# Kernel tuning notes

Hardware: AMD Instinct MI355X
Metric: run time of the kernel (lower is better)

Reference implementation:

```python
import jax, jax.numpy as jnp
import numpy as np

N = 262144          # total neurons (num_neurons * batch_size)
S = 4194304         # total synapses (~16 per neuron)
L = 8               # delay ring-buffer length (steps)
DT = 1e-4
SLOPE = 4.0
T_NOW = 0.0
# uniform per-neuron params (original stores them via _full(const))
SOMA_C, SOMA_GL, SOMA_EL = 2e-10, 1e-8, -0.070
AIS_C, AIS_GL, AIS_EL = 1e-10, 1e-8, -0.070
V_T, DELTA_T, V_SPIKE, V_RESET = -0.050, 0.002, -0.030, -0.065
G_C = 5e-9
# uniform per-synapse params (tiled constants in connect())
G_MAX, E_REV, TAU_DECAY = 1e-9, 0.0, 0.005
A_PLUS, A_MINUS, TAU_PRE, TAU_POST = 0.01, 0.012, 0.020, 0.020
ETA_BCM, TAU_RATE, TAU_THETA = 1e-4, 0.100, 1.000
W_MIN, W_MAX = 0.0, 1.0


def setup_inputs() -> dict:
    key = jax.random.key(0)
    ks = jax.random.split(key, 14)
    return {
        "external_current": 2e-10 * jax.random.normal(ks[0], (N,), jnp.float32),
        "syn_w": jax.random.uniform(ks[1], (S,), jnp.float32),
        "V_soma": SOMA_EL + 0.005 * jax.random.normal(ks[2], (N,), jnp.float32),
        "V_ais": -0.050 + 0.030 * jax.random.normal(ks[3], (N,), jnp.float32),
        "refrac_until": jnp.full((N,), -1e9, jnp.float32),
        "syn_g": 0.5 * jax.random.uniform(ks[4], (S,), jnp.float32),
        "pre_trace": jax.random.uniform(ks[5], (S,), jnp.float32),
        "post_trace": jax.random.uniform(ks[6], (S,), jnp.float32),
        "r_pre": jax.random.uniform(ks[7], (S,), jnp.float32),
        "r_post": jax.random.uniform(ks[8], (S,), jnp.float32),
        "theta_m": jax.random.uniform(ks[9], (S,), jnp.float32),
        "g_incr_buffer": jnp.zeros((L, S), jnp.float32),
        "syn_pre_idx": jax.random.randint(ks[10], (S,), 0, N, jnp.int32),
        "syn_post_idx": jax.random.randint(ks[11], (S,), 0, N, jnp.int32),
        "delay_steps": jax.random.randint(ks[12], (S,), 1, L, jnp.int32),
        "buffer_idx": 0,
    }


def reference(external_current, syn_w, V_soma, V_ais, refrac_until, syn_g,
              pre_trace, post_trace, r_pre, r_post, theta_m,
              g_incr_buffer, syn_pre_idx, syn_post_idx, delay_steps, buffer_idx):
    n = V_soma.shape[0]
    # conductance-based synaptic current, gathered from post voltage, scattered to post neurons
    i_syn = syn_g * syn_w * G_MAX * (E_REV - V_soma[syn_post_idx])
    I_syn_total = jax.ops.segment_sum(i_syn, syn_post_idx, num_segments=n)
    # two-compartment step (explicit Euler): passive soma + AdEx AIS, coupled by g_c
    dvs = (DT / SOMA_C) * (-SOMA_GL * (V_soma - SOMA_EL) + external_current
                           + I_syn_total + G_C * (V_ais - V_soma))
    exp_term = AIS_GL * DELTA_T * jnp.exp(jnp.minimum((V_ais - V_T) / DELTA_T, 20.0))
    dva = (DT / AIS_C) * (-AIS_GL * (V_ais - AIS_EL) + exp_term + G_C * (V_soma - V_ais))
    V_soma_new = V_soma + dvs
    V_ais_new = jnp.where(T_NOW < refrac_until, V_RESET, V_ais + dva)
    # spike detection with sigmoid surrogate gradient
    hard = (V_ais_new >= V_SPIKE).astype(V_ais_new.dtype)
    soft = jax.nn.sigmoid(SLOPE * (V_ais_new - V_SPIKE))
    spikes = soft + jax.lax.stop_gradient(hard - soft)
    V_ais_out = jnp.where(hard > 0, V_RESET, V_ais_new)
    # conductance: exponential decay + delayed arrivals read from ring buffer slot
    arrivals = g_incr_buffer[buffer_idx]
    syn_g_new = syn_g * jnp.exp(-DT / TAU_DECAY) + arrivals
    pre_spk = spikes[syn_pre_idx]
    post_spk = spikes[syn_post_idx]
    # schedule this step's pre-spikes at per-synapse delay slots; clear consumed slot
    rows = (buffer_idx + delay_steps) % L
    buf_new = g_incr_buffer.at[buffer_idx].set(0.0).at[rows, jnp.arange(syn_w.shape[0])].add(pre_spk)
    # STDP eligibility traces
    pre_tr = pre_trace * jnp.exp(-DT / TAU_PRE) + pre_spk
    post_tr = post_trace * jnp.exp(-DT / TAU_POST) + post_spk
    dw_stdp = A_PLUS * pre_tr * post_spk - A_MINUS * post_tr * pre_spk
    # BCM low-pass rates and sliding threshold
    r_pre_n = r_pre * jnp.exp(-DT / TAU_RATE) + pre_spk
    r_post_n = r_post * jnp.exp(-DT / TAU_RATE) + post_spk
    theta_n = theta_m + (DT / TAU_THETA) * (r_post_n * r_post_n - theta_m)
    dw_bcm = ETA_BCM * r_pre_n * r_post_n * (r_post_n - theta_n)
    w_new = jnp.clip(syn_w + dw_stdp + dw_bcm, W_MIN, W_MAX)
    return (spikes, V_soma_new, V_ais_out, syn_g_new, w_new, buf_new)
```

## Files before the change

kernel.cpp:

```cpp
#include <hip/hip_runtime.h>
#include <math.h>

#define C_DT_OVER_SOMA  500000.0f
#define C_DT_OVER_AIS   1000000.0f
#define C_SOMA_GL       1e-8f
#define C_SOMA_EL       (-0.070f)
#define C_AIS_GL        1e-8f
#define C_AIS_EL        (-0.070f)
#define C_V_T           (-0.050f)
#define C_DELTA_T       0.002f
#define C_V_SPIKE       (-0.030f)
#define C_V_RESET       (-0.065f)
#define C_G_C           5e-9f
#define C_G_MAX         1e-9f
#define C_DECAY_G       0.9801986733067553f
#define C_DECAY_TR      0.9950124791926823f
#define C_DECAY_RATE    0.9990004998333751f
#define C_DT_TAU_THETA  1e-4f
#define C_A_PLUS        0.01f
#define C_A_MINUS       0.012f
#define C_ETA_BCM       1e-4f

#define TILE_BITS   15
#define TILE_SIZE   32768
#define TILE_MASK   (TILE_SIZE - 1)
#define NTILES      8
#define KCHUNK      32
#define RING_BPR    256

typedef float fx4 __attribute__((ext_vector_type(4)));
typedef unsigned char uchar;

__device__ __forceinline__ fx4 nt_load4(const float* p) {
    return __builtin_nontemporal_load((const fx4*)p);
}
__device__ __forceinline__ void nt_store4(float* p, fx4 v) {
    __builtin_nontemporal_store(v, (fx4*)p);
}

__global__ void k_zero4(float4* __restrict__ p, int n4) {
    int i = blockIdx.x * blockDim.x + threadIdx.x;
    if (i < n4) p[i] = make_float4(0.f, 0.f, 0.f, 0.f);
}

__global__ void __launch_bounds__(512, 1)
k_scatter_tile(const float4* __restrict__ g4,
               const float4* __restrict__ w4,
               const int4*   __restrict__ post4,
               float*        __restrict__ partials,
               int S) {
    extern __shared__ float acc[];
    const int t = blockIdx.x & (NTILES - 1);
    const int k = blockIdx.x >> 3;

    for (int i = threadIdx.x; i < TILE_SIZE; i += blockDim.x)
        acc[i] = 0.0f;
    __syncthreads();

    const int cnt4  = (S / KCHUNK) / 4;
    const int base4 = k * cnt4;
    for (int j = threadIdx.x; j < cnt4; j += blockDim.x) {
        int4   p = post4[base4 + j];
        float4 g = g4[base4 + j];
        float4 w = w4[base4 + j];
        if ((p.x >> TILE_BITS) == t) atomicAdd(&acc[p.x & TILE_MASK], g.x * w.x);
        if ((p.y >> TILE_BITS) == t) atomicAdd(&acc[p.y & TILE_MASK], g.y * w.y);
        if ((p.z >> TILE_BITS) == t) atomicAdd(&acc[p.z & TILE_MASK], g.z * w.z);
        if ((p.w >> TILE_BITS) == t) atomicAdd(&acc[p.w & TILE_MASK], g.w * w.w);
    }
    __syncthreads();

    float4* dst = (float4*)(partials + (size_t)blockIdx.x * TILE_SIZE);
    const float4* src = (const float4*)acc;
    for (int i = threadIdx.x; i < TILE_SIZE / 4; i += blockDim.x)
        dst[i] = src[i];
}

template <bool FAST>
__global__ void k_neuron(const float* __restrict__ ext,
                         const float* __restrict__ Vs,
                         const float* __restrict__ Va,
                         const float* __restrict__ refrac,
                         const float* __restrict__ A,
                         float* __restrict__ spikes,
                         float* __restrict__ Vs_out,
                         float* __restrict__ Va_out,
                         int N) {
    int i = blockIdx.x * blockDim.x + threadIdx.x;
    if (i >= N) return;
    float acc = 0.0f;
    if (FAST) {
        const int t = i >> TILE_BITS;
        const int local = i & TILE_MASK;
        const float* base = A + ((size_t)t * KCHUNK) * TILE_SIZE + local;
        #pragma unroll
        for (int k = 0; k < KCHUNK; ++k) acc += base[(size_t)k * TILE_SIZE];
    } else {
        acc = A[i];
    }
    float vs = Vs[i];
    float va = Va[i];
    float I_syn = C_G_MAX * (0.0f - vs) * acc;
    float dvs = C_DT_OVER_SOMA * (-C_SOMA_GL * (vs - C_SOMA_EL) + ext[i]
                                  + I_syn + C_G_C * (va - vs));
    float xarg = fminf((va - C_V_T) / C_DELTA_T, 20.0f);
    float exp_term = C_AIS_GL * C_DELTA_T * expf(xarg);
    float dva = C_DT_OVER_AIS * (-C_AIS_GL * (va - C_AIS_EL) + exp_term
                                 + C_G_C * (vs - va));
    float vs_new = vs + dvs;
    float va_new = (0.0f < refrac[i]) ? C_V_RESET : (va + dva);
    float hard = (va_new >= C_V_SPIKE) ? 1.0f : 0.0f;
    float va_out = (hard > 0.0f) ? C_V_RESET : va_new;
    spikes[i] = hard;
    __builtin_nontemporal_store(vs_new, &Vs_out[i]);
    __builtin_nontemporal_store(va_out, &Va_out[i]);
}

__global__ void k_bits(const float* __restrict__ spikes,
                       unsigned long long* __restrict__ bits,
                       int N) {
    int i = blockIdx.x * blockDim.x + threadIdx.x;
    if (i >= N) return;
    float s = spikes[i];
    unsigned long long m = __ballot(s > 0.5f);
    if ((threadIdx.x & 63) == 0) bits[i >> 6] = m;
}

__global__ void k_scatter_gw_dev(const float4* __restrict__ g4,
                                 const float4* __restrict__ w4,
                                 const int4*   __restrict__ post4,
                                 float*        __restrict__ A,
                                 int S4) {
    int t = blockIdx.x * blockDim.x + threadIdx.x;
    if (t >= S4) return;
    float4 g = g4[t];
    float4 w = w4[t];
    int4   p = post4[t];
    unsafeAtomicAdd(&A[p.x], g.x * w.x);
    unsafeAtomicAdd(&A[p.y], g.y * w.y);
    unsafeAtomicAdd(&A[p.z], g.z * w.z);
    unsafeAtomicAdd(&A[p.w], g.w * w.w);
}

__device__ __forceinline__ float bit_gather(const unsigned* __restrict__ bits32, int idx) {
    return (float)((bits32[idx >> 5] >> (idx & 31)) & 1u);
}

__global__ void k_plast_bits(const float* __restrict__ syn_w,
                             const float* __restrict__ pre_trace,
                             const float* __restrict__ post_trace,
                             const float* __restrict__ r_pre,
                             const float* __restrict__ r_post,
                             const float* __restrict__ theta_m,
                             const int*   __restrict__ pre_idx,
                             const int*   __restrict__ post_idx,
                             const int*   __restrict__ delay,
                             const int*   __restrict__ bidx_p,
                             const unsigned* __restrict__ bits32,
                             float* __restrict__ w_out,
                             uchar* __restrict__ prerow,
                             int S) {
    int t = blockIdx.x * blockDim.x + threadIdx.x;
    int j = t * 8;
    if (j >= S) return;
    const int bidx = bidx_p[0];

    int4 pi0 = *(const int4*)(pre_idx + j);
    int4 pi1 = *(const int4*)(pre_idx + j + 4);
    int4 qi0 = *(const int4*)(post_idx + j);
    int4 qi1 = *(const int4*)(post_idx + j + 4);
    int4 dl0 = *(const int4*)(delay + j);
    int4 dl1 = *(const int4*)(delay + j + 4);

    float pre[8], post[8];
    pre[0] = bit_gather(bits32, pi0.x); pre[1] = bit_gather(bits32, pi0.y);
    pre[2] = bit_gather(bits32, pi0.z); pre[3] = bit_gather(bits32, pi0.w);
    pre[4] = bit_gather(bits32, pi1.x); pre[5] = bit_gather(bits32, pi1.y);
    pre[6] = bit_gather(bits32, pi1.z); pre[7] = bit_gather(bits32, pi1.w);
    post[0] = bit_gather(bits32, qi0.x); post[1] = bit_gather(bits32, qi0.y);
    post[2] = bit_gather(bits32, qi0.z); post[3] = bit_gather(bits32, qi0.w);
    post[4] = bit_gather(bits32, qi1.x); post[5] = bit_gather(bits32, qi1.y);
    post[6] = bit_gather(bits32, qi1.z); post[7] = bit_gather(bits32, qi1.w);

    float4 w0  = *(const float4*)(syn_w + j);
    float4 w1  = *(const float4*)(syn_w + j + 4);
    float4 pt0 = *(const float4*)(pre_trace + j);
    float4 pt1 = *(const float4*)(pre_trace + j + 4);
    float4 qt0 = *(const float4*)(post_trace + j);
    float4 qt1 = *(const float4*)(post_trace + j + 4);
    float4 rp0 = *(const float4*)(r_pre + j);
    float4 rp1 = *(const float4*)(r_pre + j + 4);
    float4 rq0 = *(const float4*)(r_post + j);
    float4 rq1 = *(const float4*)(r_post + j + 4);
    float4 th0 = *(const float4*)(theta_m + j);
    float4 th1 = *(const float4*)(theta_m + j + 4);

    float wv[8]  = {w0.x, w0.y, w0.z, w0.w, w1.x, w1.y, w1.z, w1.w};
    float ptv[8] = {pt0.x, pt0.y, pt0.z, pt0.w, pt1.x, pt1.y, pt1.z, pt1.w};
    float qtv[8] = {qt0.x, qt0.y, qt0.z, qt0.w, qt1.x, qt1.y, qt1.z, qt1.w};
    float rpv[8] = {rp0.x, rp0.y, rp0.z, rp0.w, rp1.x, rp1.y, rp1.z, rp1.w};
    float rqv[8] = {rq0.x, rq0.y, rq0.z, rq0.w, rq1.x, rq1.y, rq1.z, rq1.w};
    float thv[8] = {th0.x, th0.y, th0.z, th0.w, th1.x, th1.y, th1.z, th1.w};
    int   dlv[8] = {dl0.x, dl0.y, dl0.z, dl0.w, dl1.x, dl1.y, dl1.z, dl1.w};

    float wo[8];
    unsigned prw[8];
    #pragma unroll
    for (int k = 0; k < 8; ++k) {
        float ptr_n = ptv[k] * C_DECAY_TR + pre[k];
        float qtr_n = qtv[k] * C_DECAY_TR + post[k];
        float dw_stdp = C_A_PLUS * ptr_n * post[k] - C_A_MINUS * qtr_n * pre[k];
        float rpn = rpv[k] * C_DECAY_RATE + pre[k];
        float rqn = rqv[k] * C_DECAY_RATE + post[k];
        float thn = thv[k] + C_DT_TAU_THETA * (rqn * rqn - thv[k]);
        float dw_bcm = C_ETA_BCM * rpn * rqn * (rqn - thn);
        float wn = wv[k] + dw_stdp + dw_bcm;
        wo[k] = fminf(fmaxf(wn, 0.0f), 1.0f);
        prw[k] = (pre[k] > 0.5f) ? (unsigned)(((bidx + dlv[k]) & 7) + 1) : 0u;
    }
    fx4 a = {wo[0], wo[1], wo[2], wo[3]};
    fx4 b = {wo[4], wo[5], wo[6], wo[7]};
    nt_store4(w_out + j, a);
    nt_store4(w_out + j + 4, b);

    uint2 packed;
    packed.x = prw[0] | (prw[1] << 8) | (prw[2] << 16) | (prw[3] << 24);
    packed.y = prw[4] | (prw[5] << 8) | (prw[6] << 16) | (prw[7] << 24);
    *(uint2*)(prerow + j) = packed;
}

__global__ void k_ring_row(const float* __restrict__ gbuf,
                           const float* __restrict__ syn_g,
                           const uchar* __restrict__ prerow,
                           const int*   __restrict__ bidx_p,
                           float* __restrict__ g_out,
                           float* __restrict__ buf_out,
                           int S) {
    const int bidx = bidx_p[0];
    const int row  = blockIdx.x / RING_BPR;
    const int blk  = blockIdx.x - row * RING_BPR;
    const int span = S / RING_BPR;
    const int base = blk * span;
    const float* src = gbuf + (size_t)row * (size_t)S;
    float*       dst = buf_out + (size_t)row * (size_t)S;
    const unsigned target = (unsigned)(row + 1);
    const int step = blockDim.x * 4;

    if (row == bidx) {
        for (int off = threadIdx.x * 4; off < span; off += step) {
            const int j = base + off;
            fx4 v  = nt_load4(src + j);
            fx4 sg = *(const fx4*)(syn_g + j);
            fx4 go = sg * (float)C_DECAY_G + v;
            nt_store4(g_out + j, go);
            unsigned wd = *(const unsigned*)(prerow + j);
            fx4 z;
            z.x = ((wd        & 255u) == target) ? 1.0f : 0.0f;
            z.y = (((wd >> 8)  & 255u) == target) ? 1.0f : 0.0f;
            z.z = (((wd >> 16) & 255u) == target) ? 1.0f : 0.0f;
            z.w = (((wd >> 24)       ) == target) ? 1.0f : 0.0f;
            nt_store4(dst + j, z);
        }
    } else {
        for (int off = threadIdx.x * 4; off < span; off += step) {
            const int j = base + off;
            fx4 v = nt_load4(src + j);
            unsigned wd = *(const unsigned*)(prerow + j);
            v.x += ((wd        & 255u) == target) ? 1.0f : 0.0f;
            v.y += (((wd >> 8)  & 255u) == target) ? 1.0f : 0.0f;
            v.z += (((wd >> 16) & 255u) == target) ? 1.0f : 0.0f;
            v.w += (((wd >> 24)       ) == target) ? 1.0f : 0.0f;
            nt_store4(dst + j, v);
        }
    }
}

__global__ void k_syn_update4(const float* __restrict__ syn_g,
                              const float* __restrict__ syn_w,
                              const float* __restrict__ pre_trace,
                              const float* __restrict__ post_trace,
                              const float* __restrict__ r_pre,
                              const float* __restrict__ r_post,
                              const float* __restrict__ theta_m,
                              const float* __restrict__ gbuf,
                              const int*   __restrict__ pre_idx,
                              const int*   __restrict__ post_idx,
                              const int*   __restrict__ delay,
                              const int*   __restrict__ bidx_p,
                              const float* __restrict__ spikes,
                              float* __restrict__ g_out,
                              float* __restrict__ w_out,
                              float* __restrict__ buf_out,
                              int S, int L) {
    int t = blockIdx.x * blockDim.x + threadIdx.x;
    int j = t * 4;
    if (j >= S) return;
    const int bidx = bidx_p[0];
    int4 pi = *(const int4*)(pre_idx + j);
    int4 qi = *(const int4*)(post_idx + j);
    int4 dl = *(const int4*)(delay + j);
    float pre[4], post[4];
    pre[0] = spikes[pi.x]; pre[1] = spikes[pi.y]; pre[2] = spikes[pi.z]; pre[3] = spikes[pi.w];
    post[0] = spikes[qi.x]; post[1] = spikes[qi.y]; post[2] = spikes[qi.z]; post[3] = spikes[qi.w];
    float4 g  = *(const float4*)(syn_g + j);
    float4 w  = *(const float4*)(syn_w + j);
    float4 pt = *(const float4*)(pre_trace + j);
    float4 qt = *(const float4*)(post_trace + j);
    float4 rp = *(const float4*)(r_pre + j);
    float4 rq = *(const float4*)(r_post + j);
    float4 th = *(const float4*)(theta_m + j);
    float wv[4]  = {w.x, w.y, w.z, w.w};
    float ptv[4] = {pt.x, pt.y, pt.z, pt.w};
    float qtv[4] = {qt.x, qt.y, qt.z, qt.w};
    float rpv[4] = {rp.x, rp.y, rp.z, rp.w};
    float rqv[4] = {rq.x, rq.y, rq.z, rq.w};
    float thv[4] = {th.x, th.y, th.z, th.w};
    float wo[4];
    #pragma unroll
    for (int k = 0; k < 4; ++k) {
        float ptr_n = ptv[k] * C_DECAY_TR + pre[k];
        float qtr_n = qtv[k] * C_DECAY_TR + post[k];
        float dw_stdp = C_A_PLUS * ptr_n * post[k] - C_A_MINUS * qtr_n * pre[k];
        float rpn = rpv[k] * C_DECAY_RATE + pre[k];
        float rqn = rqv[k] * C_DECAY_RATE + post[k];
        float thn = thv[k] + C_DT_TAU_THETA * (rqn * rqn - thv[k]);
        float dw_bcm = C_ETA_BCM * rpn * rqn * (rqn - thn);
        float wn = wv[k] + dw_stdp + dw_bcm;
        wo[k] = fminf(fmaxf(wn, 0.0f), 1.0f);
    }
    float4 wo4 = {wo[0], wo[1], wo[2], wo[3]};
    *(float4*)(w_out + j) = wo4;
    int row[4];
    row[0] = (bidx + dl.x) % L;
    row[1] = (bidx + dl.y) % L;
    row[2] = (bidx + dl.z) % L;
    row[3] = (bidx + dl.w) % L;
    float gv[4] = {g.x, g.y, g.z, g.w};
    for (int r = 0; r < L; ++r) {
        float4 v = *(const float4*)(gbuf + (size_t)r * (size_t)S + j);
        float vv[4] = {v.x, v.y, v.z, v.w};
        if (r == bidx) {
            float4 gn;
            gn.x = gv[0] * C_DECAY_G + vv[0];
            gn.y = gv[1] * C_DECAY_G + vv[1];
            gn.z = gv[2] * C_DECAY_G + vv[2];
            gn.w = gv[3] * C_DECAY_G + vv[3];
            *(float4*)(g_out + j) = gn;
            vv[0] = vv[1] = vv[2] = vv[3] = 0.0f;
        }
        #pragma unroll
        for (int k = 0; k < 4; ++k)
            if (r == row[k]) vv[k] += pre[k];
        float4 ov = {vv[0], vv[1], vv[2], vv[3]};
        *(float4*)(buf_out + (size_t)r * (size_t)S + j) = ov;
    }
}

extern "C" void kernel_launch(void* const* d_in, const int* in_sizes, int n_in,
                              void* d_out, int out_size, void* d_ws, size_t ws_size,
                              hipStream_t stream) {
    const int N = in_sizes[0];
    const int S = in_sizes[1];
    const int L = in_sizes[11] / S;

    const float* ext        = (const float*)d_in[0];
    const float* syn_w      = (const float*)d_in[1];
    const float* Vs         = (const float*)d_in[2];
    const float* Va         = (const float*)d_in[3];
    const float* refrac     = (const float*)d_in[4];
    const float* syn_g      = (const float*)d_in[5];
    const float* pre_trace  = (const float*)d_in[6];
    const float* post_trace = (const float*)d_in[7];
    const float* r_pre      = (const float*)d_in[8];
    const float* r_post     = (const float*)d_in[9];
    const float* theta_m    = (const float*)d_in[10];
    const float* gbuf       = (const float*)d_in[11];
    const int*   pre_idx    = (const int*)d_in[12];
    const int*   post_idx   = (const int*)d_in[13];
    const int*   delay      = (const int*)d_in[14];
    const int*   bidx       = (const int*)d_in[15];

    float* out     = (float*)d_out;
    float* spikes  = out;
    float* Vs_out  = out + (size_t)N;
    float* Va_out  = out + (size_t)2 * N;
    float* g_out   = out + (size_t)3 * N;
    float* w_out   = out + (size_t)3 * N + (size_t)S;
    float* buf_out = out + (size_t)3 * N + (size_t)2 * S;

    float* A = (float*)d_ws;
    uchar* prerow = (uchar*)d_ws;
    unsigned long long* bits = (unsigned long long*)((char*)d_ws + ((size_t)8 << 20));

    const size_t need = (size_t)NTILES * KCHUNK * TILE_SIZE * sizeof(float);
    const bool fastScatter = (N == NTILES * TILE_SIZE) &&
                             (S % (KCHUNK * 4) == 0) &&
                             (ws_size >= need);
    const bool fastSyn = fastScatter && (L == 8) && (S % (RING_BPR * 256 * 4) == 0) &&
                         (S % 8 == 0) && (N % 256 == 0) &&
                         (((size_t)8 << 20) + N / 8 <= ws_size) && ((size_t)S <= ((size_t)8 << 20));

    const int B = 256;
    if (fastScatter) {
        k_scatter_tile<<<NTILES * KCHUNK, 512, TILE_SIZE * sizeof(float), stream>>>(
            (const float4*)syn_g, (const float4*)syn_w, (const int4*)post_idx, A, S);
        k_neuron<true><<<(N + B - 1) / B, B, 0, stream>>>(ext, Vs, Va, refrac, A,
                                                          spikes, Vs_out, Va_out, N);
    } else {
        const int S4 = S / 4;
        k_zero4<<<(N / 4 + B - 1) / B, B, 0, stream>>>((float4*)A, N / 4);
        k_scatter_gw_dev<<<(S4 + B - 1) / B, B, 0, stream>>>((const float4*)syn_g,
                                                             (const float4*)syn_w,
                                                             (const int4*)post_idx, A, S4);
        k_neuron<false><<<(N + B - 1) / B, B, 0, stream>>>(ext, Vs, Va, refrac, A,
                                                           spikes, Vs_out, Va_out, N);
    }

    if (fastSyn) {
        k_bits<<<N / B, B, 0, stream>>>(spikes, bits, N);
        const int T8 = S / 8;
        k_plast_bits<<<(T8 + B - 1) / B, B, 0, stream>>>(syn_w, pre_trace, post_trace,
                                                         r_pre, r_post, theta_m,
                                                         pre_idx, post_idx, delay, bidx,
                                                         (const unsigned*)bits,
                                                         w_out, prerow, S);
        k_ring_row<<<8 * RING_BPR, B, 0, stream>>>(gbuf, syn_g, prerow, bidx,
                                                   g_out, buf_out, S);
    } else {
        const int T4 = (S + 3) / 4;
        k_syn_update4<<<(T4 + B - 1) / B, B, 0, stream>>>(syn_g, syn_w, pre_trace, post_trace,
                                                          r_pre, r_post, theta_m, gbuf,
                                                          pre_idx, post_idx, delay, bidx,
                                                          spikes, g_out, w_out, buf_out, S, L);
    }
}
```

Measured before the change: 158.0 us.

## Stage spike bitmask in LDS, use nontemporal streaming loads, reorder scatter tile grid

The plasticity kernel now copies the whole 32 KB spike bitmask into shared memory per block, so the 16 random pre/post spike lookups hit LDS instead of global memory. Streaming per-synapse loads (indices, delays, weights, traces, syn_g, partial sums) use nontemporal hints to reduce cache pollution. The scatter-tile grid mapping is changed so consecutive blocks share a tile, with partials written to the same layout. The price is a 32 KB LDS fill per plasticity block, which may lower occupancy and add redundant global reads.

After: 181.4 us. +14.8%, slower.

```diff
diff --git a/kernel.cpp b/kernel.cpp
--- a/kernel.cpp
+++ b/kernel.cpp
@@ -27,12 +27,20 @@
 #define NTILES      8
 #define KCHUNK      32
 #define RING_BPR    256
+#define NBW         8192
 
 typedef float fx4 __attribute__((ext_vector_type(4)));
+typedef int   ix4 __attribute__((ext_vector_type(4)));
 typedef unsigned char uchar;
 
 __device__ __forceinline__ fx4 nt_load4(const float* p) {
     return __builtin_nontemporal_load((const fx4*)p);
+}
+__device__ __forceinline__ ix4 nt_loadi4(const int* p) {
+    return __builtin_nontemporal_load((const ix4*)p);
+}
+__device__ __forceinline__ float nt_loadf(const float* p) {
+    return __builtin_nontemporal_load(p);
 }
 __device__ __forceinline__ void nt_store4(float* p, fx4 v) {
     __builtin_nontemporal_store(v, (fx4*)p);
@@ -50,8 +58,8 @@
                float*        __restrict__ partials,
                int S) {
     extern __shared__ float acc[];
-    const int t = blockIdx.x & (NTILES - 1);
-    const int k = blockIdx.x >> 3;
+    const int t = blockIdx.x >> 5;
+    const int k = blockIdx.x & 31;
 
     for (int i = threadIdx.x; i < TILE_SIZE; i += blockDim.x)
         acc[i] = 0.0f;
@@ -70,10 +78,10 @@
     }
     __syncthreads();
 
-    float4* dst = (float4*)(partials + (size_t)blockIdx.x * TILE_SIZE);
+    float* dst = partials + ((size_t)t * KCHUNK + k) * TILE_SIZE;
     const float4* src = (const float4*)acc;
     for (int i = threadIdx.x; i < TILE_SIZE / 4; i += blockDim.x)
-        dst[i] = src[i];
+        ((float4*)dst)[i] = src[i];
 }
 
 template <bool FAST>
@@ -94,7 +102,7 @@
         const int local = i & TILE_MASK;
         const float* base = A + ((size_t)t * KCHUNK) * TILE_SIZE + local;
         #pragma unroll
-        for (int k = 0; k < KCHUNK; ++k) acc += base[(size_t)k * TILE_SIZE];
+        for (int k = 0; k < KCHUNK; ++k) acc += nt_loadf(base + (size_t)k * TILE_SIZE);
     } else {
         acc = A[i];
     }
@@ -142,10 +150,6 @@
     unsafeAtomicAdd(&A[p.w], g.w * w.w);
 }
 
-__device__ __forceinline__ float bit_gather(const unsigned* __restrict__ bits32, int idx) {
-    return (float)((bits32[idx >> 5] >> (idx & 31)) & 1u);
-}
-
 __global__ void k_plast_bits(const float* __restrict__ syn_w,
                              const float* __restrict__ pre_trace,
                              const float* __restrict__ post_trace,
@@ -160,40 +164,46 @@
                              float* __restrict__ w_out,
                              uchar* __restrict__ prerow,
                              int S) {
+    __shared__ unsigned sb[NBW];
+    for (int i = threadIdx.x; i < NBW; i += blockDim.x)
+        sb[i] = bits32[i];
+    __syncthreads();
+
     int t = blockIdx.x * blockDim.x + threadIdx.x;
     int j = t * 8;
     if (j >= S) return;
     const int bidx = bidx_p[0];
 
-    int4 pi0 = *(const int4*)(pre_idx + j);
-    int4 pi1 = *(const int4*)(pre_idx + j + 4);
-    int4 qi0 = *(const int4*)(post_idx + j);
-    int4 qi1 = *(const int4*)(post_idx + j + 4);
-    int4 dl0 = *(const int4*)(delay + j);
-    int4 dl1 = *(const int4*)(delay + j + 4);
+    ix4 pi0 = nt_loadi4(pre_idx + j);
+    ix4 pi1 = nt_loadi4(pre_idx + j + 4);
+    ix4 qi0 = nt_loadi4(post_idx + j);
+    ix4 qi1 = nt_loadi4(post_idx + j + 4);
+    ix4 dl0 = nt_loadi4(delay + j);
+    ix4 dl1 = nt_loadi4(delay + j + 4);
+
+    int piv[8] = {pi0.x, pi0.y, pi0.z, pi0.w, pi1.x, pi1.y, pi1.z, pi1.w};
+    int qiv[8] = {qi0.x, qi0.y, qi0.z, qi0.w, qi1.x, qi1.y, qi1.z, qi1.w};
+    int dlv[8] = {dl0.x, dl0.y, dl0.z, dl0.w, dl1.x, dl1.y, dl1.z, dl1.w};
 
     float pre[8], post[8];
-    pre[0] = bit_gather(bits32, pi0.x); pre[1] = bit_gather(bits32, pi0.y);
-    pre[2] = bit_gather(bits32, pi0.z); pre[3] = bit_gather(bits32, pi0.w);
-    pre[4] = bit_gather(bits32, pi1.x); pre[5] = bit_gather(bits32, pi1.y);
-    pre[6] = bit_gather(bits32, pi1.z); pre[7] = bit_gather(bits32, pi1.w);
-    post[0] = bit_gather(bits32, qi0.x); post[1] = bit_gather(bits32, qi0.y);
-    post[2] = bit_gather(bits32, qi0.z); post[3] = bit_gather(bits32, qi0.w);
-    post[4] = bit_gather(bits32, qi1.x); post[5] = bit_gather(bits32, qi1.y);
-    post[6] = bit_gather(bits32, qi1.z); post[7] = bit_gather(bits32, qi1.w);
-
-    float4 w0  = *(const float4*)(syn_w + j);
-    float4 w1  = *(const float4*)(syn_w + j + 4);
-    float4 pt0 = *(const float4*)(pre_trace + j);
-    float4 pt1 = *(const float4*)(pre_trace + j + 4);
-    float4 qt0 = *(const float4*)(post_trace + j);
-    float4 qt1 = *(const float4*)(post_trace + j + 4);
-    float4 rp0 = *(const float4*)(r_pre + j);
-    float4 rp1 = *(const float4*)(r_pre + j + 4);
-    float4 rq0 = *(const float4*)(r_post + j);
-    float4 rq1 = *(const float4*)(r_post + j + 4);
-    float4 th0 = *(const float4*)(theta_m + j);
-    float4 th1 = *(const float4*)(theta_m + j + 4);
+    #pragma unroll
+    for (int k = 0; k < 8; ++k) {
+        pre[k]  = (float)((sb[piv[k] >> 5] >> (piv[k] & 31)) & 1u);
+        post[k] = (float)((sb[qiv[k] >> 5] >> (qiv[k] & 31)) & 1u);
+    }
+
+    fx4 w0  = nt_load4(syn_w + j);
+    fx4 w1  = nt_load4(syn_w + j + 4);
+    fx4 pt0 = nt_load4(pre_trace + j);
+    fx4 pt1 = nt_load4(pre_trace + j + 4);
+    fx4 qt0 = nt_load4(post_trace + j);
+    fx4 qt1 = nt_load4(post_trace + j + 4);
+    fx4 rp0 = nt_load4(r_pre + j);
+    fx4 rp1 = nt_load4(r_pre + j + 4);
+    fx4 rq0 = nt_load4(r_post + j);
+    fx4 rq1 = nt_load4(r_post + j + 4);
+    fx4 th0 = nt_load4(theta_m + j);
+    fx4 th1 = nt_load4(theta_m + j + 4);
 
     float wv[8]  = {w0.x, w0.y, w0.z, w0.w, w1.x, w1.y, w1.z, w1.w};
     float ptv[8] = {pt0.x, pt0.y, pt0.z, pt0.w, pt1.x, pt1.y, pt1.z, pt1.w};
@@ -201,7 +211,6 @@
     float rpv[8] = {rp0.x, rp0.y, rp0.z, rp0.w, rp1.x, rp1.y, rp1.z, rp1.w};
     float rqv[8] = {rq0.x, rq0.y, rq0.z, rq0.w, rq1.x, rq1.y, rq1.z, rq1.w};
     float thv[8] = {th0.x, th0.y, th0.z, th0.w, th1.x, th1.y, th1.z, th1.w};
-    int   dlv[8] = {dl0.x, dl0.y, dl0.z, dl0.w, dl1.x, dl1.y, dl1.z, dl1.w};
 
     float wo[8];
     unsigned prw[8];
@@ -250,7 +259,7 @@
         for (int off = threadIdx.x * 4; off < span; off += step) {
             const int j = base + off;
             fx4 v  = nt_load4(src + j);
-            fx4 sg = *(const fx4*)(syn_g + j);
+            fx4 sg = nt_load4(syn_g + j);
             fx4 go = sg * (float)C_DECAY_G + v;
             nt_store4(g_out + j, go);
             unsigned wd = *(const unsigned*)(prerow + j);
```
